# Kernel tuning notes

Hardware: AMD Instinct MI355X
Metric: run time of the kernel (lower is better)

The kernel has to match this reference:

```python
import jax, jax.numpy as jnp
import numpy as np

B, N, E, D_IN, D_OUT = 16, 2048, 65536, 256, 256


def setup_inputs() -> dict:
    key = jax.random.key(0)
    k1, k2, k3 = jax.random.split(key, 3)
    node_features = jax.random.normal(k1, (B, N, D_IN), dtype=jnp.float32)
    edge_indices = jax.random.randint(k2, (B, 2, E), 0, N, dtype=jnp.int64)
    W = jax.random.normal(k3, (D_OUT, 2 * D_IN), dtype=jnp.float32) * (1.0 / np.sqrt(2 * D_IN))
    b = jnp.zeros((D_OUT,), dtype=jnp.float32)
    return {"node_features": node_features, "edge_indices": edge_indices, "W": W, "b": b}


def reference(node_features, edge_indices, W, b):
    # node_features: [B, N, D]; edge_indices: [B, 2, E] (src row 0, dst row 1)
    n_nodes = node_features.shape[1]
    src = edge_indices[:, 0, :]  # [B, E]
    dst = edge_indices[:, 1, :]  # [B, E]
    # gather source-node features per edge: [B, E, D]
    gathered = jnp.take_along_axis(node_features, src[:, :, None], axis=1)

    def per_graph(feats_g, dst_g):
        s = jax.ops.segment_sum(feats_g, dst_g, num_segments=n_nodes)          # [N, D]
        c = jax.ops.segment_sum(jnp.ones_like(dst_g, dtype=feats_g.dtype),
                                dst_g, num_segments=n_nodes)                    # [N]
        return s / jnp.maximum(c, 1.0)[:, None]  # mean; 0 for isolated nodes

    neighbor_agg = jax.vmap(per_graph)(gathered, dst)            # [B, N, D]
    combined = jnp.concatenate([node_features, neighbor_agg], axis=-1)  # [B, N, 2D]
    return jnp.einsum('bnd,od->bno', combined, W) + b
```

## Files before the change

### kernel.cpp

```cpp
#include <hip/hip_runtime.h>
#include <hip/hip_bf16.h>

#define BATCH 16
#define NNODE 2048
#define NEDGE 65536
#define DIN   256
#define DOUT  256
#define KDIM  512
#define SUB   16
#define ESUB  (NEDGE/SUB)

typedef __attribute__((ext_vector_type(8))) short short8;
typedef __attribute__((ext_vector_type(8))) ushort ushort8;
typedef __attribute__((ext_vector_type(4))) float f32x4;

__device__ __forceinline__ ushort f2bf(float f) {
    union { float f; unsigned u; } v; v.f = f;
    unsigned u = v.u;
    unsigned r = (u + 0x7fffu + ((u >> 16) & 1u)) >> 16;
    return (ushort)r;
}

__device__ __forceinline__ int q8(float x) {
    float c = fminf(fmaxf(x * 16.0f, -127.0f), 127.0f);
    return (int)rintf(c);
}

#define ASYNC_COPY16(gsrc, ldst) \
    __builtin_amdgcn_global_load_lds((const __attribute__((address_space(1))) void*)(gsrc), \
                                     (__attribute__((address_space(3))) void*)(ldst), 16, 0, 0)

__global__ __launch_bounds__(256) void prep_kernel(
        const float* __restrict__ X, const float* __restrict__ W,
        const int* __restrict__ E,
        int* __restrict__ partial,
        ushort* __restrict__ Xbf, unsigned char* __restrict__ Xi8,
        ushort* __restrict__ Wbf) {
    int bid = blockIdx.x;
    int t = threadIdx.x;
    if (bid < 256) {
        __shared__ int hist[NNODE];
        int b = bid & 15, sub = bid >> 4;
#pragma unroll
        for (int j = 0; j < 8; ++j) hist[t + j * 256] = 0;
        __syncthreads();
        const int4* dsts = reinterpret_cast<const int4*>(
            E + (size_t)b * 2 * NEDGE + NEDGE + sub * ESUB);
#pragma unroll
        for (int j = 0; j < 4; ++j) {
            int4 d = dsts[j * 256 + t];
            atomicAdd(&hist[d.x], 1);
            atomicAdd(&hist[d.y], 1);
            atomicAdd(&hist[d.z], 1);
            atomicAdd(&hist[d.w], 1);
        }
        __syncthreads();
        int* pb = partial + ((size_t)b * SUB + sub) * NNODE;
#pragma unroll
        for (int j = 0; j < 8; ++j) pb[t + j * 256] = hist[t + j * 256];
    } else if (bid < 4352) {
        size_t i = (size_t)(bid - 256) * 256 + t;
        const float4* p = reinterpret_cast<const float4*>(X + i * 8);
        float4 u = p[0], v = p[1];
        ushort4 o0 = { f2bf(u.x), f2bf(u.y), f2bf(u.z), f2bf(u.w) };
        ushort4 o1 = { f2bf(v.x), f2bf(v.y), f2bf(v.z), f2bf(v.w) };
        *reinterpret_cast<ushort4*>(Xbf + i * 8)     = o0;
        *reinterpret_cast<ushort4*>(Xbf + i * 8 + 4) = o1;
        unsigned q0 = (q8(u.x) & 255) | ((q8(u.y) & 255) << 8) |
                      ((q8(u.z) & 255) << 16) | ((unsigned)(q8(u.w) & 255) << 24);
        unsigned q1 = (q8(v.x) & 255) | ((q8(v.y) & 255) << 8) |
                      ((q8(v.z) & 255) << 16) | ((unsigned)(q8(v.w) & 255) << 24);
        uint2 q = { q0, q1 };
        *reinterpret_cast<uint2*>(Xi8 + i * 8) = q;
    } else {
        size_t i = (size_t)(bid - 4352) * 256 + t;
        const float4* p = reinterpret_cast<const float4*>(W + i * 8);
        float4 u = p[0], v = p[1];
        ushort4 o0 = { f2bf(u.x), f2bf(u.y), f2bf(u.z), f2bf(u.w) };
        ushort4 o1 = { f2bf(v.x), f2bf(v.y), f2bf(v.z), f2bf(v.w) };
        *reinterpret_cast<ushort4*>(Wbf + i * 8)     = o0;
        *reinterpret_cast<ushort4*>(Wbf + i * 8 + 4) = o1;
    }
}

__global__ __launch_bounds__(256) void fillscan_kernel(
        const int* __restrict__ E,
        const int* __restrict__ partial,
        int* __restrict__ counts, int* __restrict__ cursor,
        int* __restrict__ srcIdx) {
    __shared__ int cur[NNODE];
    __shared__ int tsum[256];
    int bid = blockIdx.x;
    int t = threadIdx.x;
    int b = bid & 15, sub = bid >> 4;
    const int* pb = partial + (size_t)b * SUB * NNODE;

    int tot[8] = {}, pre[8] = {};
    for (int k = 0; k < SUB; ++k) {
        const int4* p = reinterpret_cast<const int4*>(pb + k * NNODE + t * 8);
        int4 a = p[0], c = p[1];
        if (k < sub) {
            pre[0] += a.x; pre[1] += a.y; pre[2] += a.z; pre[3] += a.w;
            pre[4] += c.x; pre[5] += c.y; pre[6] += c.z; pre[7] += c.w;
        }
        tot[0] += a.x; tot[1] += a.y; tot[2] += a.z; tot[3] += a.w;
        tot[4] += c.x; tot[5] += c.y; tot[6] += c.z; tot[7] += c.w;
    }
    int s = 0;
#pragma unroll
    for (int j = 0; j < 8; ++j) s += tot[j];
    tsum[t] = s;
    __syncthreads();
    for (int off = 1; off < 256; off <<= 1) {
        int v = (t >= off) ? tsum[t - off] : 0;
        __syncthreads();
        tsum[t] += v;
        __syncthreads();
    }
    int run = (t == 0) ? 0 : tsum[t - 1];
    bool writer = (sub == 0);
    int base = b * NNODE + t * 8;
#pragma unroll
    for (int j = 0; j < 8; ++j) {
        cur[t * 8 + j] = run + pre[j];
        if (writer) { counts[base + j] = tot[j]; cursor[base + j] = run; }
        run += tot[j];
    }
    __syncthreads();

    const int* eb = E + (size_t)b * 2 * NEDGE;
    const int4* srcs = reinterpret_cast<const int4*>(eb + sub * ESUB);
    const int4* dsts = reinterpret_cast<const int4*>(eb + NEDGE + sub * ESUB);
    int* sb = srcIdx + (size_t)b * NEDGE;
#pragma unroll
    for (int j = 0; j < 4; ++j) {
        int4 sv = srcs[j * 256 + t];
        int4 dv = dsts[j * 256 + t];
        sb[atomicAdd(&cur[dv.x], 1)] = sv.x;
        sb[atomicAdd(&cur[dv.y], 1)] = sv.y;
        sb[atomicAdd(&cur[dv.z], 1)] = sv.z;
        sb[atomicAdd(&cur[dv.w], 1)] = sv.w;
    }
}

__global__ __launch_bounds__(256) void aggregate_kernel(
        const unsigned char* __restrict__ Xi8,
        const int* __restrict__ srcIdx,
        const int* __restrict__ cursor,
        const int* __restrict__ counts,
        ushort* __restrict__ Gbf) {
    int bid = blockIdx.x;
    int blk = (bid & 7) * 1024 + (bid >> 3);
    int wave = threadIdx.x >> 6;
    int lane = threadIdx.x & 63;
    int half = lane >> 5;
    int f0 = (lane & 31) * 8;
    int node = blk * 4 + wave;
    int b = node >> 11;
    int deg = counts[node];
    int start = cursor[node];
    const unsigned char* xb = Xi8 + (size_t)b * NNODE * DIN;
    const int* sidx = srcIdx + (size_t)b * NEDGE + start;

    unsigned aA0 = 0, aA1 = 0, aB0 = 0, aB1 = 0;
#define ACC8(v) do {                                                          \
        unsigned wx = (v).x ^ 0x80808080u, wy = (v).y ^ 0x80808080u;          \
        aA0 += wx & 0x00FF00FFu;  aA1 += (wx >> 8) & 0x00FF00FFu;             \
        aB0 += wy & 0x00FF00FFu;  aB1 += (wy >> 8) & 0x00FF00FFu;             \
    } while (0)

    int i = 0;
    for (; i + 16 <= deg; i += 16) {
        int s[8];
#pragma unroll
        for (int u = 0; u < 8; ++u) s[u] = sidx[i + 2 * u + half];
        uint2 v[8];
#pragma unroll
        for (int u = 0; u < 8; ++u)
            v[u] = *reinterpret_cast<const uint2*>(xb + (size_t)s[u] * DIN + f0);
#pragma unroll
        for (int u = 0; u < 8; ++u) ACC8(v[u]);
    }
    for (; i + 8 <= deg; i += 8) {
        int s0 = sidx[i + 0 + half], s1 = sidx[i + 2 + half];
        int s2 = sidx[i + 4 + half], s3 = sidx[i + 6 + half];
        uint2 v0 = *reinterpret_cast<const uint2*>(xb + (size_t)s0 * DIN + f0);
        uint2 v1 = *reinterpret_cast<const uint2*>(xb + (size_t)s1 * DIN + f0);
        uint2 v2 = *reinterpret_cast<const uint2*>(xb + (size_t)s2 * DIN + f0);
        uint2 v3 = *reinterpret_cast<const uint2*>(xb + (size_t)s3 * DIN + f0);
        ACC8(v0); ACC8(v1); ACC8(v2); ACC8(v3);
    }
    for (; i + 2 <= deg; i += 2) {
        int s0 = sidx[i + half];
        uint2 v0 = *reinterpret_cast<const uint2*>(xb + (size_t)s0 * DIN + f0);
        ACC8(v0);
    }
    if (i < deg && half == 0) {
        int s0 = sidx[i];
        uint2 v0 = *reinterpret_cast<const uint2*>(xb + (size_t)s0 * DIN + f0);
        ACC8(v0);
    }
#undef ACC8
    aA0 += (unsigned)__shfl_xor((int)aA0, 32, 64);
    aA1 += (unsigned)__shfl_xor((int)aA1, 32, 64);
    aB0 += (unsigned)__shfl_xor((int)aB0, 32, 64);
    aB1 += (unsigned)__shfl_xor((int)aB1, 32, 64);

    if (half == 0) {
        float sc = 1.0f / (16.0f * (float)max(deg, 1));
        float bias = 128.0f * (float)deg;
        float f[8];
        f[0] = ((float)(int)(aA0 & 0xFFFFu) - bias) * sc;
        f[2] = ((float)(int)(aA0 >> 16)     - bias) * sc;
        f[1] = ((float)(int)(aA1 & 0xFFFFu) - bias) * sc;
        f[3] = ((float)(int)(aA1 >> 16)     - bias) * sc;
        f[4] = ((float)(int)(aB0 & 0xFFFFu) - bias) * sc;
        f[6] = ((float)(int)(aB0 >> 16)     - bias) * sc;
        f[5] = ((float)(int)(aB1 & 0xFFFFu) - bias) * sc;
        f[7] = ((float)(int)(aB1 >> 16)     - bias) * sc;
        ushort8 o;
#pragma unroll
        for (int j = 0; j < 8; ++j) o[j] = f2bf(f[j]);
        *reinterpret_cast<ushort8*>(Gbf + (size_t)node * DIN + f0) = o;
    }
}

__global__ __launch_bounds__(256) void gemm_kernel(
        const ushort* __restrict__ Xbf,
        const ushort* __restrict__ Gbf,
        const ushort* __restrict__ Wbf,
        const float* __restrict__ bias,
        float* __restrict__ out) {
    __shared__ ushort As[2][128 * 32];
    __shared__ ushort Bs[2][128 * 32];
    const int tid = threadIdx.x;
    const int wid = tid >> 6, lane = tid & 63;

    int orig = blockIdx.x;
    int logical = (orig & 7) * 64 + (orig >> 3);
    int bx = logical >> 1;
    int by = logical & 1;
    const int rowBase = bx * 128;
    const int colBase = by * 128;
    const int wm = wid >> 1, wn = wid & 1;

    f32x4 acc[4][4] = {};

    const int lr = lane >> 2;
    const int lk = (((lane & 3) ^ ((lane >> 3) & 3)) * 8);

    const ushort* Arow = Xbf + (size_t)rowBase * DIN;
    const ushort* Grow = Gbf + (size_t)rowBase * DIN;
    const ushort* Brow = Wbf + (size_t)colBase * KDIM;
    const int r0 = wid * 16 + lr;

#define STAGE(k0, buf) do {                                                   \
        const ushort* Ab = ((k0) < DIN) ? (Arow + (k0)) : (Grow + ((k0) - DIN)); \
        const ushort* Bb = Brow + (k0);                                       \
        ASYNC_COPY16(Ab + (size_t)r0 * DIN + lk,          &As[buf][wid * 512]);       \
        ASYNC_COPY16(Ab + (size_t)(r0 + 64) * DIN + lk,   &As[buf][2048 + wid * 512]);\
        ASYNC_COPY16(Bb + (size_t)r0 * KDIM + lk,         &Bs[buf][wid * 512]);       \
        ASYNC_COPY16(Bb + (size_t)(r0 + 64) * KDIM + lk,  &Bs[buf][2048 + wid * 512]);\
    } while (0)

    const int fl = lane & 15;
    const int fc = ((lane >> 4) ^ ((fl >> 1) & 3)) * 8;

    STAGE(0, 0);
    int cur = 0;
    for (int t = 0; t < 16; ++t) {
        if (t < 15) {
            STAGE((t + 1) * 32, cur ^ 1);
            asm volatile("s_waitcnt vmcnt(4)" ::: "memory");
        } else {
            asm volatile("s_waitcnt vmcnt(0)" ::: "memory");
        }
        __builtin_amdgcn_s_barrier();

        short8 a[4], b[4];
#pragma unroll
        for (int m = 0; m < 4; ++m)
            a[m] = *reinterpret_cast<const short8*>(
                &As[cur][(wm * 64 + m * 16 + fl) * 32 + fc]);
#pragma unroll
        for (int n = 0; n < 4; ++n)
            b[n] = *reinterpret_cast<const short8*>(
                &Bs[cur][(wn * 64 + n * 16 + fl) * 32 + fc]);
#pragma unroll
        for (int m = 0; m < 4; ++m)
#pragma unroll
            for (int n = 0; n < 4; ++n)
                acc[m][n] = __builtin_amdgcn_mfma_f32_16x16x32_bf16(
                    a[m], b[n], acc[m][n], 0, 0, 0);
        __builtin_amdgcn_s_barrier();
        cur ^= 1;
    }
#undef STAGE

    const int cl = lane & 15, rq = lane >> 4;
#pragma unroll
    for (int n = 0; n < 4; ++n) {
        int col = colBase + wn * 64 + n * 16 + cl;
        float bv = bias[col];
#pragma unroll
        for (int m = 0; m < 4; ++m) {
            int r0o = rowBase + wm * 64 + m * 16 + rq * 4;
#pragma unroll
            for (int j = 0; j < 4; ++j)
                out[(size_t)(r0o + j) * DOUT + col] = acc[m][n][j] + bv;
        }
    }
}

extern "C" void kernel_launch(void* const* d_in, const int* in_sizes, int n_in,
                              void* d_out, int out_size, void* d_ws, size_t ws_size,
                              hipStream_t stream) {
    const float* X    = (const float*)d_in[0];
    const int*   E    = (const int*)d_in[1];
    const float* W    = (const float*)d_in[2];
    const float* bias = (const float*)d_in[3];
    float* out = (float*)d_out;

    char* ws = (char*)d_ws;
    ushort* Xbf  = (ushort*)ws;
    ushort* Gbf  = Xbf + (size_t)BATCH * NNODE * DIN;
    ushort* Wbf  = Gbf + (size_t)BATCH * NNODE * DIN;
    int* counts  = (int*)(Wbf + (size_t)DOUT * KDIM);
    int* cursor  = counts + BATCH * NNODE;
    int* srcIdx  = cursor + BATCH * NNODE;
    unsigned char* Xi8 = (unsigned char*)(srcIdx + (size_t)BATCH * NEDGE);
    int* partial = (int*)Gbf;

    prep_kernel<<<4416, 256, 0, stream>>>(X, W, E, partial, Xbf, Xi8, Wbf);

    fillscan_kernel<<<256, 256, 0, stream>>>(E, partial, counts, cursor, srcIdx);

    aggregate_kernel<<<(BATCH * NNODE) / 4, 256, 0, stream>>>(
        Xi8, srcIdx, cursor, counts, Gbf);

    dim3 ggrid(512);
    gemm_kernel<<<ggrid, 256, 0, stream>>>(Xbf, Gbf, Wbf, bias, out);
}
```

Baseline: 67.05 us.

## Widen aggregation gathers to 16-byte loads and triple-buffer GEMM tiles

In the aggregation kernel, each lane now gathers 16 int8 features with a uint4 load instead of 8, and four edges are processed in parallel per wave (lane groups of 16), reduced with two shuffles. The tail is handled by padding with the zero-offset pattern. Separately, the GEMM moves from double to triple buffering of LDS tiles with a two-stage prefetch depth, to hide more global-load latency. LDS use per block increases, which may reduce occupancy, and the aggregation adds more shuffle work.

After: 66.91 us. No clear change (-0.2%).

```diff
diff --git a/kernel.cpp b/kernel.cpp
--- a/kernel.cpp
+++ b/kernel.cpp
@@ -153,8 +153,9 @@
     int blk = (bid & 7) * 1024 + (bid >> 3);
     int wave = threadIdx.x >> 6;
     int lane = threadIdx.x & 63;
-    int half = lane >> 5;
-    int f0 = (lane & 31) * 8;
+    int q = lane >> 4;
+    int l16 = lane & 15;
+    int f0 = l16 * 16;
     int node = blk * 4 + wave;
     int b = node >> 11;
     int deg = counts[node];
@@ -162,66 +163,72 @@
     const unsigned char* xb = Xi8 + (size_t)b * NNODE * DIN;
     const int* sidx = srcIdx + (size_t)b * NEDGE + start;
 
-    unsigned aA0 = 0, aA1 = 0, aB0 = 0, aB1 = 0;
-#define ACC8(v) do {                                                          \
-        unsigned wx = (v).x ^ 0x80808080u, wy = (v).y ^ 0x80808080u;          \
-        aA0 += wx & 0x00FF00FFu;  aA1 += (wx >> 8) & 0x00FF00FFu;             \
-        aB0 += wy & 0x00FF00FFu;  aB1 += (wy >> 8) & 0x00FF00FFu;             \
+    unsigned a0 = 0, a1 = 0, a2 = 0, a3 = 0, a4 = 0, a5 = 0, a6 = 0, a7 = 0;
+#define M16 0x00FF00FFu
+#define ACC16(v) do {                                                         \
+        unsigned w0 = (v).x ^ 0x80808080u, w1 = (v).y ^ 0x80808080u;          \
+        unsigned w2 = (v).z ^ 0x80808080u, w3 = (v).w ^ 0x80808080u;          \
+        a0 += w0 & M16;  a1 += (w0 >> 8) & M16;                               \
+        a2 += w1 & M16;  a3 += (w1 >> 8) & M16;                               \
+        a4 += w2 & M16;  a5 += (w2 >> 8) & M16;                               \
+        a6 += w3 & M16;  a7 += (w3 >> 8) & M16;                               \
     } while (0)
 
     int i = 0;
     for (; i + 16 <= deg; i += 16) {
-        int s[8];
-#pragma unroll
-        for (int u = 0; u < 8; ++u) s[u] = sidx[i + 2 * u + half];
-        uint2 v[8];
-#pragma unroll
-        for (int u = 0; u < 8; ++u)
-            v[u] = *reinterpret_cast<const uint2*>(xb + (size_t)s[u] * DIN + f0);
-#pragma unroll
-        for (int u = 0; u < 8; ++u) ACC8(v[u]);
-    }
-    for (; i + 8 <= deg; i += 8) {
-        int s0 = sidx[i + 0 + half], s1 = sidx[i + 2 + half];
-        int s2 = sidx[i + 4 + half], s3 = sidx[i + 6 + half];
-        uint2 v0 = *reinterpret_cast<const uint2*>(xb + (size_t)s0 * DIN + f0);
-        uint2 v1 = *reinterpret_cast<const uint2*>(xb + (size_t)s1 * DIN + f0);
-        uint2 v2 = *reinterpret_cast<const uint2*>(xb + (size_t)s2 * DIN + f0);
-        uint2 v3 = *reinterpret_cast<const uint2*>(xb + (size_t)s3 * DIN + f0);
-        ACC8(v0); ACC8(v1); ACC8(v2); ACC8(v3);
-    }
-    for (; i + 2 <= deg; i += 2) {
-        int s0 = sidx[i + half];
-        uint2 v0 = *reinterpret_cast<const uint2*>(xb + (size_t)s0 * DIN + f0);
-        ACC8(v0);
-    }
-    if (i < deg && half == 0) {
-        int s0 = sidx[i];
-        uint2 v0 = *reinterpret_cast<const uint2*>(xb + (size_t)s0 * DIN + f0);
-        ACC8(v0);
-    }
-#undef ACC8
-    aA0 += (unsigned)__shfl_xor((int)aA0, 32, 64);
-    aA1 += (unsigned)__shfl_xor((int)aA1, 32, 64);
-    aB0 += (unsigned)__shfl_xor((int)aB0, 32, 64);
-    aB1 += (unsigned)__shfl_xor((int)aB1, 32, 64);
-
-    if (half == 0) {
+        int s0 = sidx[i + q], s1 = sidx[i + 4 + q];
+        int s2 = sidx[i + 8 + q], s3 = sidx[i + 12 + q];
+        uint4 v0 = *reinterpret_cast<const uint4*>(xb + (size_t)s0 * DIN + f0);
+        uint4 v1 = *reinterpret_cast<const uint4*>(xb + (size_t)s1 * DIN + f0);
+        uint4 v2 = *reinterpret_cast<const uint4*>(xb + (size_t)s2 * DIN + f0);
+        uint4 v3 = *reinterpret_cast<const uint4*>(xb + (size_t)s3 * DIN + f0);
+        ACC16(v0); ACC16(v1); ACC16(v2); ACC16(v3);
+    }
+    for (; i < deg; i += 4) {
+        int e = i + q;
+        uint4 v = { 0x80808080u, 0x80808080u, 0x80808080u, 0x80808080u };
+        if (e < deg) {
+            int s0 = sidx[e];
+            v = *reinterpret_cast<const uint4*>(xb + (size_t)s0 * DIN + f0);
+        }
+        ACC16(v);
+    }
+#undef ACC16
+    a0 += (unsigned)__shfl_xor((int)a0, 16, 64); a0 += (unsigned)__shfl_xor((int)a0, 32, 64);
+    a1 += (unsigned)__shfl_xor((int)a1, 16, 64); a1 += (unsigned)__shfl_xor((int)a1, 32, 64);
+    a2 += (unsigned)__shfl_xor((int)a2, 16, 64); a2 += (unsigned)__shfl_xor((int)a2, 32, 64);
+    a3 += (unsigned)__shfl_xor((int)a3, 16, 64); a3 += (unsigned)__shfl_xor((int)a3, 32, 64);
+    a4 += (unsigned)__shfl_xor((int)a4, 16, 64); a4 += (unsigned)__shfl_xor((int)a4, 32, 64);
+    a5 += (unsigned)__shfl_xor((int)a5, 16, 64); a5 += (unsigned)__shfl_xor((int)a5, 32, 64);
+    a6 += (unsigned)__shfl_xor((int)a6, 16, 64); a6 += (unsigned)__shfl_xor((int)a6, 32, 64);
+    a7 += (unsigned)__shfl_xor((int)a7, 16, 64); a7 += (unsigned)__shfl_xor((int)a7, 32, 64);
+
+    if (q == 0) {
         float sc = 1.0f / (16.0f * (float)max(deg, 1));
         float bias = 128.0f * (float)deg;
-        float f[8];
-        f[0] = ((float)(int)(aA0 & 0xFFFFu) - bias) * sc;
-        f[2] = ((float)(int)(aA0 >> 16)     - bias) * sc;
-        f[1] = ((float)(int)(aA1 & 0xFFFFu) - bias) * sc;
-        f[3] = ((float)(int)(aA1 >> 16)     - bias) * sc;
-        f[4] = ((float)(int)(aB0 & 0xFFFFu) - bias) * sc;
-        f[6] = ((float)(int)(aB0 >> 16)     - bias) * sc;
-        f[5] = ((float)(int)(aB1 & 0xFFFFu) - bias) * sc;
-        f[7] = ((float)(int)(aB1 >> 16)     - bias) * sc;
-        ushort8 o;
-#pragma unroll
-        for (int j = 0; j < 8; ++j) o[j] = f2bf(f[j]);
-        *reinterpret_cast<ushort8*>(Gbf + (size_t)node * DIN + f0) = o;
+        float f[16];
+        f[ 0] = ((float)(int)(a0 & 0xFFFFu) - bias) * sc;
+        f[ 2] = ((float)(int)(a0 >> 16)     - bias) * sc;
+        f[ 1] = ((float)(int)(a1 & 0xFFFFu) - bias) * sc;
+        f[ 3] = ((float)(int)(a1 >> 16)     - bias) * sc;
+        f[ 4] = ((float)(int)(a2 & 0xFFFFu) - bias) * sc;
+        f[ 6] = ((float)(int)(a2 >> 16)     - bias) * sc;
+        f[ 5] = ((float)(int)(a3 & 0xFFFFu) - bias) * sc;
+        f[ 7] = ((float)(int)(a3 >> 16)     - bias) * sc;
+        f[ 8] = ((float)(int)(a4 & 0xFFFFu) - bias) * sc;
+        f[10] = ((float)(int)(a4 >> 16)     - bias) * sc;
+        f[ 9] = ((float)(int)(a5 & 0xFFFFu) - bias) * sc;
+        f[11] = ((float)(int)(a5 >> 16)     - bias) * sc;
+        f[12] = ((float)(int)(a6 & 0xFFFFu) - bias) * sc;
+        f[14] = ((float)(int)(a6 >> 16)     - bias) * sc;
+        f[13] = ((float)(int)(a7 & 0xFFFFu) - bias) * sc;
+        f[15] = ((float)(int)(a7 >> 16)     - bias) * sc;
+        ushort8 o0, o1;
+#pragma unroll
+        for (int j = 0; j < 8; ++j) { o0[j] = f2bf(f[j]); o1[j] = f2bf(f[j + 8]); }
+        ushort* gp = Gbf + (size_t)node * DIN + f0;
+        *reinterpret_cast<ushort8*>(gp)     = o0;
+        *reinterpret_cast<ushort8*>(gp + 8) = o1;
     }
 }
 
@@ -231,8 +238,8 @@
         const ushort* __restrict__ Wbf,
         const float* __restrict__ bias,
         float* __restrict__ out) {
-    __shared__ ushort As[2][128 * 32];
-    __shared__ ushort Bs[2][128 * 32];
+    __shared__ ushort As[3][128 * 32];
+    __shared__ ushort Bs[3][128 * 32];
     const int tid = threadIdx.x;
     const int wid = tid >> 6, lane = tid & 63;
 
@@ -267,10 +274,13 @@
     const int fc = ((lane >> 4) ^ ((fl >> 1) & 3)) * 8;
 
     STAGE(0, 0);
-    int cur = 0;
+    STAGE(32, 1);
     for (int t = 0; t < 16; ++t) {
-        if (t < 15) {
-            STAGE((t + 1) * 32, cur ^ 1);
+        const int bt = t % 3;
+        if (t + 2 < 16) {
+            STAGE((t + 2) * 32, (t + 2) % 3);
+            asm volatile("s_waitcnt vmcnt(8)" ::: "memory");
+        } else if (t + 1 < 16) {
             asm volatile("s_waitcnt vmcnt(4)" ::: "memory");
         } else {
             asm volatile("s_waitcnt vmcnt(0)" ::: "memory");
@@ -281,11 +291,11 @@
 #pragma unroll
         for (int m = 0; m < 4; ++m)
             a[m] = *reinterpret_cast<const short8*>(
-                &As[cur][(wm * 64 + m * 16 + fl) * 32 + fc]);
+                &As[bt][(wm * 64 + m * 16 + fl) * 32 + fc]);
 #pragma unroll
         for (int n = 0; n < 4; ++n)
             b[n] = *reinterpret_cast<const short8*>(
-                &Bs[cur][(wn * 64 + n * 16 + fl) * 32 + fc]);
+                &Bs[bt][(wn * 64 + n * 16 + fl) * 32 + fc]);
 #pragma unroll
         for (int m = 0; m < 4; ++m)
 #pragma unroll
@@ -293,7 +303,6 @@
                 acc[m][n] = __builtin_amdgcn_mfma_f32_16x16x32_bf16(
                     a[m], b[n], acc[m][n], 0, 0, 0);
         __builtin_amdgcn_s_barrier();
-        cur ^= 1;
     }
 #undef STAGE
 
```
